# Kernel optimization log

Hardware: AMD Instinct MI355X
Metric: run time of the kernel (lower is better)

Reference implementation:

```python
import jax, jax.numpy as jnp
import numpy as np

B = 8192
N_IN = 1024
N_OUT = 1024
IN_OUT = N_IN + N_OUT


def setup_inputs() -> dict:
    key = jax.random.key(0)
    ks = jax.random.split(key, 11)
    s = 1.0 / np.sqrt(IN_OUT)  # nn.Linear default init scale
    inp = {
        "x": jax.random.normal(ks[0], (B, N_IN), dtype=jnp.float32),
        "out_tm1": jax.random.normal(ks[1], (B, N_OUT), dtype=jnp.float32),
        "state_tm1": jax.random.normal(ks[2], (B, N_OUT), dtype=jnp.float32),
        "Wf": jax.random.uniform(ks[3], (IN_OUT, N_OUT), jnp.float32, -s, s),
        "bf": jax.random.uniform(ks[4], (N_OUT,), jnp.float32, -s, s),
        "Wi": jax.random.uniform(ks[5], (IN_OUT, N_OUT), jnp.float32, -s, s),
        "bi": jax.random.uniform(ks[6], (N_OUT,), jnp.float32, -s, s),
        "Wc": jax.random.uniform(ks[7], (IN_OUT, N_OUT), jnp.float32, -s, s),
        "bc": jax.random.uniform(ks[8], (N_OUT,), jnp.float32, -s, s),
        "Wo": jax.random.uniform(ks[9], (IN_OUT, N_OUT), jnp.float32, -s, s),
        "bo": jax.random.uniform(ks[10], (N_OUT,), jnp.float32, -s, s),
    }
    return inp


def reference(x, out_tm1, state_tm1, Wf, bf, Wi, bi, Wc, bc, Wo, bo):
    xh = jnp.concatenate((x, out_tm1), axis=-1)  # [B, n_in+n_out]
    f = jax.nn.sigmoid(xh @ Wf + bf)             # forget gate
    i = jax.nn.sigmoid(xh @ Wi + bi)             # input gate
    c = jnp.tanh(xh @ Wc + bc)                   # candidates
    o = jax.nn.sigmoid(xh @ Wo + bo)             # output gate
    new_state = state_tm1 * f + i * c
    output_t = o * jnp.tanh(new_state)
    return (output_t, new_state)
```

## Files before the change

### kernel.cpp

```cpp
#include <hip/hip_runtime.h>

#define B_DIM 8192
#define NOUT  1024
#define KDIM  2048

typedef __bf16 bf16x8 __attribute__((ext_vector_type(8)));
typedef float  f32x4  __attribute__((ext_vector_type(4)));

__device__ __forceinline__ unsigned short f2bf(float f) {
  unsigned int u = __float_as_uint(f);
  u += 0x7fff + ((u >> 16) & 1);
  return (unsigned short)(u >> 16);
}
__device__ __forceinline__ float sigmoid_f(float x) {
  return 1.0f / (1.0f + __expf(-x));
}
__device__ __forceinline__ float tanh_f(float x) {
  return 1.0f - 2.0f / (__expf(2.0f * x) + 1.0f);
}
__device__ __forceinline__ void gload_lds16(const void* g, void* l) {
  __builtin_amdgcn_global_load_lds(
      (const __attribute__((address_space(1))) void*)g,
      (__attribute__((address_space(3))) void*)l, 16, 0, 0);
}

__device__ __forceinline__ int cimap(int g, int n) {
  return ((n >> 6) << 8) | ((g >> 1) << 7) | (((n >> 4) & 3) << 5) |
         ((g & 1) << 4) | (n & 15);
}

__global__ void pack_xh_kernel(const float* __restrict__ x,
                               const float* __restrict__ h,
                               unsigned short* __restrict__ xh) {
  const long total = (long)B_DIM * KDIM / 4;
  for (long i = (long)blockIdx.x * blockDim.x + threadIdx.x; i < total;
       i += (long)gridDim.x * blockDim.x) {
    long e = i * 4;
    int b = (int)(e >> 11);
    int c = (int)(e & 2047);
    float4 v = (c < 1024)
        ? *reinterpret_cast<const float4*>(x + (long)b * 1024 + c)
        : *reinterpret_cast<const float4*>(h + (long)b * 1024 + (c - 1024));
    ushort4 o;
    o.x = f2bf(v.x); o.y = f2bf(v.y); o.z = f2bf(v.z); o.w = f2bf(v.w);
    *reinterpret_cast<ushort4*>(xh + e) = o;
  }
}

__global__ void transpose_w_kernel(const float* __restrict__ Wf,
                                   const float* __restrict__ Wi,
                                   const float* __restrict__ Wc,
                                   const float* __restrict__ Wo,
                                   unsigned short* __restrict__ wt) {
  __shared__ float tile[32][33];
  const int g = blockIdx.z;
  const float* W = (g == 0) ? Wf : (g == 1) ? Wi : (g == 2) ? Wc : Wo;
  const int n0 = blockIdx.x * 32;
  const int k0 = blockIdx.y * 32;
  const int tx = threadIdx.x, ty = threadIdx.y;
#pragma unroll
  for (int r = ty; r < 32; r += 8)
    tile[r][tx] = W[(long)(k0 + r) * NOUT + n0 + tx];
  __syncthreads();
#pragma unroll
  for (int r = ty; r < 32; r += 8) {
    int ci = cimap(g, n0 + r);
    wt[(long)ci * KDIM + k0 + tx] = f2bf(tile[tx][r]);
  }
}

#define BAR()   { __builtin_amdgcn_s_barrier(); __builtin_amdgcn_sched_barrier(0); }
#define VM6()   { asm volatile("s_waitcnt vmcnt(6)" ::: "memory"); }
#define VM2()   { asm volatile("s_waitcnt vmcnt(2)" ::: "memory"); }
#define VM0()   { asm volatile("s_waitcnt vmcnt(0)" ::: "memory"); }

__device__ __forceinline__ void stage_half(const char* g, long grow0, int kt,
                                           char* ldsm, int base,
                                           int wave, int lane) {
  const int rsub = lane >> 3;
  const int scol = (((lane & 7) ^ rsub) << 4);
  const long rowb = (grow0 + wave * 8 + rsub) * 4096 + (long)kt * 128 + scol;
  gload_lds16(g + rowb,               ldsm + base + wave * 1024);
  gload_lds16(g + rowb + 64L * 4096,  ldsm + base + 8192 + wave * 1024);
}

#define LOAD_AF(BUF, MQ)                                                    \
  _Pragma("unroll") for (int mi = 0; mi < 4; ++mi) {                        \
    af[mi][0] = *reinterpret_cast<const bf16x8*>(                           \
        baseA0 + (BUF)*32768 + (MQ)*16384 + mi*2048);                       \
    af[mi][1] = *reinterpret_cast<const bf16x8*>(                           \
        baseA1 + (BUF)*32768 + (MQ)*16384 + mi*2048);                       \
  }

#define LOAD_BQ(BUF, NQ, DST)                                               \
  _Pragma("unroll") for (int ni = 0; ni < 2; ++ni) {                        \
    DST[ni][0] = *reinterpret_cast<const bf16x8*>(                          \
        baseB0 + (BUF)*32768 + (NQ)*16384 + ni*2048);                       \
    DST[ni][1] = *reinterpret_cast<const bf16x8*>(                          \
        baseB1 + (BUF)*32768 + (NQ)*16384 + ni*2048);                       \
  }

#define MFMA16(MQ, NQ, BQ)                                                  \
  _Pragma("unroll") for (int mi = 0; mi < 4; ++mi)                          \
  _Pragma("unroll") for (int ni = 0; ni < 2; ++ni)                          \
  _Pragma("unroll") for (int s = 0; s < 2; ++s)                             \
    acc[MQ][NQ][mi][ni] = __builtin_amdgcn_mfma_f32_16x16x32_bf16(          \
        af[mi][s], BQ[ni][s], acc[MQ][NQ][mi][ni], 0, 0, 0);

__global__ __launch_bounds__(512, 2)
void lstm_gemm_kernel(const unsigned short* __restrict__ xh,
                      const unsigned short* __restrict__ wt,
                      const float* __restrict__ state,
                      const float* __restrict__ bfp,
                      const float* __restrict__ bip,
                      const float* __restrict__ bcp,
                      const float* __restrict__ bop,
                      float* __restrict__ out) {
  __shared__ __attribute__((aligned(128))) char lds[131072];

  const int tid  = threadIdx.x;
  const int wave = tid >> 6;
  const int lane = tid & 63;
  const int wm = wave >> 2;
  const int wn = wave & 3;

  int wg = blockIdx.y * 16 + blockIdx.x;
  wg = (wg & 7) * 64 + (wg >> 3);
  const int  bm = wg >> 4;
  const int  bn = wg & 15;
  const long m0 = (long)bm * 256;
  const long n0 = (long)bn * 256;

  const int lrow  = lane & 15;
  const int csw   = (lane & 7) << 4;
  const int ck    = (lane >> 4) << 4;
  const int colA0 = ck ^ csw;
  const int colA1 = (64 | ck) ^ csw;

  const char* baseA0 = lds + (wm * 64 + lrow) * 128 + colA0;
  const char* baseA1 = lds + (wm * 64 + lrow) * 128 + colA1;
  const char* baseB0 = lds + 65536 + (wn * 32 + lrow) * 128 + colA0;
  const char* baseB1 = lds + 65536 + (wn * 32 + lrow) * 128 + colA1;

  const char* xh_b = (const char*)xh;
  const char* wt_b = (const char*)wt;

  stage_half(xh_b, m0,        0, lds, 0,             wave, lane);
  stage_half(wt_b, n0,        0, lds, 65536,         wave, lane);
  stage_half(wt_b, n0 + 128,  0, lds, 65536 + 16384, wave, lane);
  stage_half(xh_b, m0 + 128,  0, lds, 16384,         wave, lane);

  f32x4 acc[2][2][4][2] = {};
  bf16x8 af[4][2];
  bf16x8 bq0[2][2];
  bf16x8 bq1[2][2];

  VM0();
  BAR();

  for (int t = 0; t < 32; t += 2) {
    const int k1  = t + 1;
    const int k2c = (t + 2 > 31) ? 31 : t + 2;

    stage_half(xh_b, m0,       k1, lds, 32768,         wave, lane);
    stage_half(wt_b, n0,       k1, lds, 65536 + 32768, wave, lane);
    stage_half(wt_b, n0 + 128, k1, lds, 65536 + 32768 + 16384, wave, lane);
    LOAD_AF(0, 0) LOAD_BQ(0, 0, bq0) LOAD_BQ(0, 1, bq1)
    VM6(); BAR();
    __builtin_amdgcn_s_setprio(1);
    MFMA16(0, 0, bq0) MFMA16(0, 1, bq1)
    __builtin_amdgcn_s_setprio(0);
    stage_half(xh_b, m0 + 128, k1, lds, 32768 + 16384, wave, lane);
    LOAD_AF(0, 1)
    VM2(); BAR();
    __builtin_amdgcn_s_setprio(1);
    MFMA16(1, 1, bq1) MFMA16(1, 0, bq0)
    __builtin_amdgcn_s_setprio(0);

    stage_half(xh_b, m0,       k2c, lds, 0,             wave, lane);
    stage_half(wt_b, n0,       k2c, lds, 65536,         wave, lane);
    stage_half(wt_b, n0 + 128, k2c, lds, 65536 + 16384, wave, lane);
    LOAD_AF(1, 0) LOAD_BQ(1, 0, bq0) LOAD_BQ(1, 1, bq1)
    VM6(); BAR();
    __builtin_amdgcn_s_setprio(1);
    MFMA16(0, 0, bq0) MFMA16(0, 1, bq1)
    __builtin_amdgcn_s_setprio(0);
    stage_half(xh_b, m0 + 128, k2c, lds, 16384, wave, lane);
    LOAD_AF(1, 1)
    VM2(); BAR();
    __builtin_amdgcn_s_setprio(1);
    MFMA16(1, 1, bq1) MFMA16(1, 0, bq0)
    __builtin_amdgcn_s_setprio(0);
  }
  VM0();

  const int   nout = bn * 64 + wn * 16 + lrow;
  const int   rsub4 = (lane >> 4) << 2;
  const float bfv = bfp[nout], biv = bip[nout];
  const float bcv = bcp[nout], bov = bop[nout];
  float* out2 = out + (long)B_DIM * NOUT;
#pragma unroll
  for (int mq = 0; mq < 2; ++mq)
#pragma unroll
    for (int mi = 0; mi < 4; ++mi)
#pragma unroll
      for (int v = 0; v < 4; ++v) {
        const long row = m0 + mq * 128 + wm * 64 + mi * 16 + rsub4 + v;
        float fg = sigmoid_f(acc[mq][0][mi][0][v] + bfv);
        float ig = sigmoid_f(acc[mq][0][mi][1][v] + biv);
        float cg = tanh_f   (acc[mq][1][mi][0][v] + bcv);
        float og = sigmoid_f(acc[mq][1][mi][1][v] + bov);
        float st = state[row * NOUT + nout];
        float ns = st * fg + ig * cg;
        out [row * NOUT + nout] = og * tanh_f(ns);
        out2[row * NOUT + nout] = ns;
      }
}

extern "C" void kernel_launch(void* const* d_in, const int* in_sizes, int n_in,
                              void* d_out, int out_size, void* d_ws, size_t ws_size,
                              hipStream_t stream) {
  const float* x     = (const float*)d_in[0];
  const float* h     = (const float*)d_in[1];
  const float* state = (const float*)d_in[2];
  const float* Wf    = (const float*)d_in[3];
  const float* bfp   = (const float*)d_in[4];
  const float* Wi    = (const float*)d_in[5];
  const float* bip   = (const float*)d_in[6];
  const float* Wc    = (const float*)d_in[7];
  const float* bcp   = (const float*)d_in[8];
  const float* Wo    = (const float*)d_in[9];
  const float* bop   = (const float*)d_in[10];
  float* out = (float*)d_out;

  unsigned short* xh = (unsigned short*)d_ws;
  unsigned short* wt = (unsigned short*)((char*)d_ws + (size_t)B_DIM * KDIM * 2);

  hipLaunchKernelGGL(pack_xh_kernel, dim3(2048), dim3(256), 0, stream, x, h, xh);
  hipLaunchKernelGGL(transpose_w_kernel, dim3(NOUT / 32, KDIM / 32, 4),
                     dim3(32, 8), 0, stream, Wf, Wi, Wc, Wo, wt);
  hipLaunchKernelGGL(lstm_gemm_kernel, dim3(16, 32), dim3(512), 0, stream,
                     xh, wt, state, bfp, bip, bcp, bop, out);
}
```

Baseline: 153.1 us.

## Load B operand fragments directly from global into registers, halve LDS

The weight (B) tiles are no longer staged through LDS. Each wave now loads its B fragments straight from global memory into registers, and the LDS buffer shrinks from 128 KB to 64 KB. Wait counts are adjusted to cover the extra outstanding global loads. This removes the LDS traffic and capacity spent on B and may allow higher occupancy. The cost is that the four wn-waves sharing each wm row each fetch the same B data from global, and the global loads land directly in the MFMA dependency path with less latency hiding.

Measured after the change: 237.5 us. 55.1% more time.

```diff
diff --git a/kernel.cpp b/kernel.cpp
--- a/kernel.cpp
+++ b/kernel.cpp
@@ -70,7 +70,7 @@
 }
 
 #define BAR()   { __builtin_amdgcn_s_barrier(); __builtin_amdgcn_sched_barrier(0); }
-#define VM6()   { asm volatile("s_waitcnt vmcnt(6)" ::: "memory"); }
+#define VM10()  { asm volatile("s_waitcnt vmcnt(10)" ::: "memory"); }
 #define VM2()   { asm volatile("s_waitcnt vmcnt(2)" ::: "memory"); }
 #define VM0()   { asm volatile("s_waitcnt vmcnt(0)" ::: "memory"); }
 
@@ -92,12 +92,10 @@
         baseA1 + (BUF)*32768 + (MQ)*16384 + mi*2048);                       \
   }
 
-#define LOAD_BQ(BUF, NQ, DST)                                               \
-  _Pragma("unroll") for (int ni = 0; ni < 2; ++ni) {                        \
-    DST[ni][0] = *reinterpret_cast<const bf16x8*>(                          \
-        baseB0 + (BUF)*32768 + (NQ)*16384 + ni*2048);                       \
-    DST[ni][1] = *reinterpret_cast<const bf16x8*>(                          \
-        baseB1 + (BUF)*32768 + (NQ)*16384 + ni*2048);                       \
+#define LOAD_BQG(T, P0, P1, DST)                                            \
+  _Pragma("unroll") for (int s = 0; s < 2; ++s) {                           \
+    DST[0][s] = *reinterpret_cast<const bf16x8*>(P0 + (long)(T)*128 + s*64);\
+    DST[1][s] = *reinterpret_cast<const bf16x8*>(P1 + (long)(T)*128 + s*64);\
   }
 
 #define MFMA16(MQ, NQ, BQ)                                                  \
@@ -116,7 +114,7 @@
                       const float* __restrict__ bcp,
                       const float* __restrict__ bop,
                       float* __restrict__ out) {
-  __shared__ __attribute__((aligned(128))) char lds[131072];
+  __shared__ __attribute__((aligned(128))) char lds[65536];
 
   const int tid  = threadIdx.x;
   const int wave = tid >> 6;
@@ -139,34 +137,36 @@
 
   const char* baseA0 = lds + (wm * 64 + lrow) * 128 + colA0;
   const char* baseA1 = lds + (wm * 64 + lrow) * 128 + colA1;
-  const char* baseB0 = lds + 65536 + (wn * 32 + lrow) * 128 + colA0;
-  const char* baseB1 = lds + 65536 + (wn * 32 + lrow) * 128 + colA1;
 
   const char* xh_b = (const char*)xh;
   const char* wt_b = (const char*)wt;
 
-  stage_half(xh_b, m0,        0, lds, 0,             wave, lane);
-  stage_half(wt_b, n0,        0, lds, 65536,         wave, lane);
-  stage_half(wt_b, n0 + 128,  0, lds, 65536 + 16384, wave, lane);
-  stage_half(xh_b, m0 + 128,  0, lds, 16384,         wave, lane);
+  const char* bgbase = wt_b + (long)(n0 + wn * 32 + lrow) * 4096 + (ck);
+  const char* bg00 = bgbase;
+  const char* bg01 = bgbase + 16L * 4096;
+  const char* bg10 = bgbase + 128L * 4096;
+  const char* bg11 = bgbase + 144L * 4096;
+
+  stage_half(xh_b, m0,        0, lds, 0,     wave, lane);
+  stage_half(xh_b, m0 + 128,  0, lds, 16384, wave, lane);
 
   f32x4 acc[2][2][4][2] = {};
   bf16x8 af[4][2];
   bf16x8 bq0[2][2];
   bf16x8 bq1[2][2];
 
-  VM0();
+  VM2();
   BAR();
 
   for (int t = 0; t < 32; t += 2) {
     const int k1  = t + 1;
     const int k2c = (t + 2 > 31) ? 31 : t + 2;
 
-    stage_half(xh_b, m0,       k1, lds, 32768,         wave, lane);
-    stage_half(wt_b, n0,       k1, lds, 65536 + 32768, wave, lane);
-    stage_half(wt_b, n0 + 128, k1, lds, 65536 + 32768 + 16384, wave, lane);
-    LOAD_AF(0, 0) LOAD_BQ(0, 0, bq0) LOAD_BQ(0, 1, bq1)
-    VM6(); BAR();
+    LOAD_BQG(t, bg00, bg01, bq0)
+    LOAD_BQG(t, bg10, bg11, bq1)
+    stage_half(xh_b, m0, k1, lds, 32768, wave, lane);
+    LOAD_AF(0, 0)
+    VM10(); BAR();
     __builtin_amdgcn_s_setprio(1);
     MFMA16(0, 0, bq0) MFMA16(0, 1, bq1)
     __builtin_amdgcn_s_setprio(0);
@@ -177,11 +177,11 @@
     MFMA16(1, 1, bq1) MFMA16(1, 0, bq0)
     __builtin_amdgcn_s_setprio(0);
 
-    stage_half(xh_b, m0,       k2c, lds, 0,             wave, lane);
-    stage_half(wt_b, n0,       k2c, lds, 65536,         wave, lane);
-    stage_half(wt_b, n0 + 128, k2c, lds, 65536 + 16384, wave, lane);
-    LOAD_AF(1, 0) LOAD_BQ(1, 0, bq0) LOAD_BQ(1, 1, bq1)
-    VM6(); BAR();
+    LOAD_BQG(k1, bg00, bg01, bq0)
+    LOAD_BQG(k1, bg10, bg11, bq1)
+    stage_half(xh_b, m0, k2c, lds, 0, wave, lane);
+    LOAD_AF(1, 0)
+    VM10(); BAR();
     __builtin_amdgcn_s_setprio(1);
     MFMA16(0, 0, bq0) MFMA16(0, 1, bq1)
     __builtin_amdgcn_s_setprio(0);
```

## Restructure GEMM main loop into 4-phase interleaved prefetch schedule per k-tile

Applied to the files above, without the earlier changes.

Replaces the two-phase per-k-tile schedule with a four-phase schedule. Each phase issues one global-to-LDS stage and the LDS fragment loads for the next MFMA quadrant, then runs one 16-MFMA block, with barriers between phases. The prologue now prefetches one extra k-tile so three tiles are in flight, and waits use lgkmcnt/vmcnt counts tuned to the new issue order. The goal is to spread memory traffic evenly between MFMA blocks and hide load latency. The cost is more barriers per tile, and buffer reuse is harder to verify.

Result: slower. 157.9 us (+3.2%).

```diff
diff --git a/kernel.cpp b/kernel.cpp
--- a/kernel.cpp
+++ b/kernel.cpp
@@ -70,8 +70,8 @@
 }
 
 #define BAR()   { __builtin_amdgcn_s_barrier(); __builtin_amdgcn_sched_barrier(0); }
+#define LGKM8() { asm volatile("s_waitcnt lgkmcnt(8)" ::: "memory"); }
 #define VM6()   { asm volatile("s_waitcnt vmcnt(6)" ::: "memory"); }
-#define VM2()   { asm volatile("s_waitcnt vmcnt(2)" ::: "memory"); }
 #define VM0()   { asm volatile("s_waitcnt vmcnt(0)" ::: "memory"); }
 
 __device__ __forceinline__ void stage_half(const char* g, long grow0, int kt,
@@ -101,11 +101,34 @@
   }
 
 #define MFMA16(MQ, NQ, BQ)                                                  \
+  __builtin_amdgcn_s_setprio(1);                                            \
   _Pragma("unroll") for (int mi = 0; mi < 4; ++mi)                          \
   _Pragma("unroll") for (int ni = 0; ni < 2; ++ni)                          \
   _Pragma("unroll") for (int s = 0; s < 2; ++s)                             \
     acc[MQ][NQ][mi][ni] = __builtin_amdgcn_mfma_f32_16x16x32_bf16(          \
-        af[mi][s], BQ[ni][s], acc[MQ][NQ][mi][ni], 0, 0, 0);
+        af[mi][s], BQ[ni][s], acc[MQ][NQ][mi][ni], 0, 0, 0);                \
+  __builtin_amdgcn_s_setprio(0);
+
+#define KTILE(BUF, KA1, KN)                                                 \
+                                                                    \
+  LOAD_AF(BUF, 0) LOAD_BQ(BUF, 0, bq0)                                      \
+  stage_half(xh_b, m0 + 128, (KA1), lds, (1-(BUF))*32768 + 16384, wave, lane);\
+  LGKM8(); BAR();                                                           \
+  MFMA16(0, 0, bq0) BAR();                                                  \
+                                                                    \
+  LOAD_BQ(BUF, 1, bq1)                                                      \
+  stage_half(xh_b, m0, (KN), lds, (BUF)*32768, wave, lane);                 \
+  BAR();                                                                    \
+  MFMA16(0, 1, bq1) BAR();                                                  \
+                                                                    \
+  LOAD_AF(BUF, 1)                                                           \
+  stage_half(wt_b, n0, (KN), lds, 65536 + (BUF)*32768, wave, lane);         \
+  BAR();                                                                    \
+  MFMA16(1, 1, bq1) BAR();                                                  \
+                                                                    \
+  stage_half(wt_b, n0 + 128, (KN), lds, 65536 + (BUF)*32768 + 16384, wave, lane);\
+  VM6(); BAR();                                                             \
+  MFMA16(1, 0, bq0) BAR();
 
 __global__ __launch_bounds__(512, 2)
 void lstm_gemm_kernel(const unsigned short* __restrict__ xh,
@@ -149,48 +172,23 @@
   stage_half(wt_b, n0,        0, lds, 65536,         wave, lane);
   stage_half(wt_b, n0 + 128,  0, lds, 65536 + 16384, wave, lane);
   stage_half(xh_b, m0 + 128,  0, lds, 16384,         wave, lane);
+  stage_half(xh_b, m0,        1, lds, 32768,                 wave, lane);
+  stage_half(wt_b, n0,        1, lds, 65536 + 32768,         wave, lane);
+  stage_half(wt_b, n0 + 128,  1, lds, 65536 + 32768 + 16384, wave, lane);
 
   f32x4 acc[2][2][4][2] = {};
   bf16x8 af[4][2];
   bf16x8 bq0[2][2];
   bf16x8 bq1[2][2];
 
-  VM0();
+  VM6();
   BAR();
 
   for (int t = 0; t < 32; t += 2) {
-    const int k1  = t + 1;
     const int k2c = (t + 2 > 31) ? 31 : t + 2;
-
-    stage_half(xh_b, m0,       k1, lds, 32768,         wave, lane);
-    stage_half(wt_b, n0,       k1, lds, 65536 + 32768, wave, lane);
-    stage_half(wt_b, n0 + 128, k1, lds, 65536 + 32768 + 16384, wave, lane);
-    LOAD_AF(0, 0) LOAD_BQ(0, 0, bq0) LOAD_BQ(0, 1, bq1)
-    VM6(); BAR();
-    __builtin_amdgcn_s_setprio(1);
-    MFMA16(0, 0, bq0) MFMA16(0, 1, bq1)
-    __builtin_amdgcn_s_setprio(0);
-    stage_half(xh_b, m0 + 128, k1, lds, 32768 + 16384, wave, lane);
-    LOAD_AF(0, 1)
-    VM2(); BAR();
-    __builtin_amdgcn_s_setprio(1);
-    MFMA16(1, 1, bq1) MFMA16(1, 0, bq0)
-    __builtin_amdgcn_s_setprio(0);
-
-    stage_half(xh_b, m0,       k2c, lds, 0,             wave, lane);
-    stage_half(wt_b, n0,       k2c, lds, 65536,         wave, lane);
-    stage_half(wt_b, n0 + 128, k2c, lds, 65536 + 16384, wave, lane);
-    LOAD_AF(1, 0) LOAD_BQ(1, 0, bq0) LOAD_BQ(1, 1, bq1)
-    VM6(); BAR();
-    __builtin_amdgcn_s_setprio(1);
-    MFMA16(0, 0, bq0) MFMA16(0, 1, bq1)
-    __builtin_amdgcn_s_setprio(0);
-    stage_half(xh_b, m0 + 128, k2c, lds, 16384, wave, lane);
-    LOAD_AF(1, 1)
-    VM2(); BAR();
-    __builtin_amdgcn_s_setprio(1);
-    MFMA16(1, 1, bq1) MFMA16(1, 0, bq0)
-    __builtin_amdgcn_s_setprio(0);
+    const int k3c = (t + 3 > 31) ? 31 : t + 3;
+    KTILE(0, t + 1, k2c)
+    KTILE(1, k2c, k3c)
   }
   VM0();
 
```
